# Performance work log

Hardware: AMD Instinct MI355X
Metric: run time of the kernel (lower is better)

The kernel has to match this reference:

```python
import math
import jax, jax.numpy as jnp
import numpy as np

N_HEADS = 8
EPS = 1e-6


def setup_inputs() -> dict:
    key = jax.random.key(0)
    k0, k1, k2, k3, k4 = jax.random.split(key, 5)
    B, T, E = 2, 1024, 512
    s = 1.0 / math.sqrt(E)
    x = jax.random.normal(k0, (B, T, E), dtype=jnp.float32)
    w_qkv = jax.random.normal(k1, (3 * E, E), dtype=jnp.float32) * s
    b_qkv = jax.random.normal(k2, (3 * E,), dtype=jnp.float32) * s
    w_out = jax.random.normal(k3, (E, E), dtype=jnp.float32) * s
    b_out = jax.random.normal(k4, (E,), dtype=jnp.float32) * s
    return {"x": x, "w_qkv": w_qkv, "b_qkv": b_qkv, "w_out": w_out, "b_out": b_out}


def reference(x, w_qkv, b_qkv, w_out, b_out):
    B, T, C = x.shape
    H = N_HEADS
    d = C // H

    qkv = x @ w_qkv.T + b_qkv                      # [B,T,3C]
    q, k, v = jnp.split(qkv, 3, axis=-1)

    def to_heads(t):
        return t.reshape(B, T, H, d).transpose(0, 2, 1, 3).astype(jnp.float32)  # [B,H,T,d]

    q, k, v = to_heads(q), to_heads(k), to_heads(v)

    pos = jnp.arange(T, dtype=jnp.float32)
    ang = (math.pi / 2) * pos / T
    cos_w = jnp.cos(ang)[None, None, :, None]      # [1,1,T,1]
    sin_w = jnp.sin(ang)[None, None, :, None]

    q_prime = jax.nn.relu(q)
    k_prime = jax.nn.relu(k)
    q_cos, q_sin = q_prime * cos_w, q_prime * sin_w
    k_cos, k_sin = k_prime * cos_w, k_prime * sin_w

    # causal linear attention via cumulative outer products (cosFormer)
    kv_cos_cs = jnp.cumsum(jnp.einsum('bhtd,bhte->bhtde', k_cos, v), axis=2)
    context = jnp.einsum('bhtd,bhtde->bhte', q_cos, kv_cos_cs)
    kv_sin_cs = jnp.cumsum(jnp.einsum('bhtd,bhte->bhtde', k_sin, v), axis=2)
    context = context + jnp.einsum('bhtd,bhtde->bhte', q_sin, kv_sin_cs)

    norm = (jnp.einsum('bhtd,bhtd->bht', q_cos, jnp.cumsum(k_cos, axis=2))
            + jnp.einsum('bhtd,bhtd->bht', q_sin, jnp.cumsum(k_sin, axis=2)))
    out = context / (norm[..., None] + EPS)        # [B,H,T,d]

    out = out.astype(x.dtype).transpose(0, 2, 1, 3).reshape(B, T, C)
    return out @ w_out.T + b_out
```

## Files before the change

kernel.cpp:

```cpp
#include <hip/hip_runtime.h>

typedef __bf16 bf16_t;
typedef __bf16 bf16x4 __attribute__((ext_vector_type(4)));
typedef __bf16 bf16x8 __attribute__((ext_vector_type(8)));
typedef float f32x4 __attribute__((ext_vector_type(4)));

#define T_SEQ 1024
#define EMB   512
#define NH    8
#define HD    64
#define BATCH 2
#define NBH   (BATCH*NH)
#define CHUNK 64
#define NCHUNK (T_SEQ/CHUNK)
#define NBLK  (NBH*NCHUNK)
#define LDA   72


__global__ __launch_bounds__(256) void cvt3_kernel(
    const float* __restrict__ x, const float* __restrict__ wq,
    const float* __restrict__ wo,
    bf16_t* __restrict__ xb, bf16_t* __restrict__ wqb, bf16_t* __restrict__ wob)
{
    int i = blockIdx.x * 256 + threadIdx.x;
    const float* s; bf16_t* d; int off;
    if (i < 262144)      { s = x;  d = xb;  off = i; }
    else if (i < 458752) { s = wq; d = wqb; off = i - 262144; }
    else                 { s = wo; d = wob; off = i - 458752; }
    float4 v = ((const float4*)s)[off];
    bf16x4 o;
    o[0] = (bf16_t)v.x; o[1] = (bf16_t)v.y;
    o[2] = (bf16_t)v.z; o[3] = (bf16_t)v.w;
    ((bf16x4*)d)[off] = o;
}

__global__ __launch_bounds__(64) void qkv_gemm_kernel(
    const bf16_t* __restrict__ X, const bf16_t* __restrict__ W,
    const float* __restrict__ bias,
    bf16_t* __restrict__ qq, bf16_t* __restrict__ kk, bf16_t* __restrict__ vv)
{
    const int lane = threadIdx.x;
    const int rsel = lane & 15;
    const int koff = (lane >> 4) * 8;
    const int m0 = blockIdx.x * 64;
    const int n0 = blockIdx.y * 64;
    f32x4 acc[4][4] = {};
    const bf16_t* Ap = X + (m0 + rsel) * EMB + koff;
    const bf16_t* Bp = W + (n0 + rsel) * EMB + koff;
#pragma unroll 4
    for (int k0 = 0; k0 < EMB; k0 += 32) {
        bf16x8 af[4], bfr[4];
        for (int i = 0; i < 4; ++i)
            af[i] = *(const bf16x8*)(Ap + i * 16 * EMB + k0);
        for (int j = 0; j < 4; ++j)
            bfr[j] = *(const bf16x8*)(Bp + j * 16 * EMB + k0);
        for (int i = 0; i < 4; ++i)
            for (int j = 0; j < 4; ++j)
                acc[i][j] = __builtin_amdgcn_mfma_f32_16x16x32_bf16(
                    af[i], bfr[j], acc[i][j], 0, 0, 0);
    }
    for (int j = 0; j < 4; ++j) {
        const int n = n0 + j * 16 + rsel;
        const float bn = bias[n];
        const int sec = n >> 9;
        const int c = n & 511;
        const int h = c >> 6, e = c & 63;
        for (int i = 0; i < 4; ++i) {
            const int mb = m0 + i * 16 + (lane >> 4) * 4;
            for (int r = 0; r < 4; ++r) {
                int m = mb + r;
                int b = m >> 10, t = m & 1023;
                float val = acc[i][j][r] + bn;
                int di = ((b * NH + h) * T_SEQ + t) * HD + e;
                if (sec == 0) {
                    qq[di] = (bf16_t)fmaxf(val, 0.f);
                } else if (sec == 1) {
                    kk[di] = (bf16_t)fmaxf(val, 0.f);
                } else {
                    vv[di] = (bf16_t)val;
                }
            }
        }
    }
}

__global__ __launch_bounds__(256) void chunk_sum_kernel(
    const bf16_t* __restrict__ kk, const bf16_t* __restrict__ vv,
    bf16_t* __restrict__ Ssc, bf16_t* __restrict__ Sss,
    float* __restrict__ zc, float* __restrict__ zs)
{
    const int blk = blockIdx.x;
    const int ch = blk & 15;
    __shared__ __align__(16) bf16_t sk[CHUNK * HD];
    __shared__ __align__(16) bf16_t sv[CHUNK * HD];
    __shared__ float cwt[CHUNK], swt[CHUNK];
    const int base = blk * CHUNK * HD;
    for (int i = threadIdx.x; i < CHUNK * HD / 8; i += 256) {
        ((uint4*)sk)[i] = ((const uint4*)(kk + base))[i];
        ((uint4*)sv)[i] = ((const uint4*)(vv + base))[i];
    }
    if (threadIdx.x < CHUNK) {
        int tg = ch * CHUNK + threadIdx.x;
        float ang = 1.5707963267948966f * (float)tg * (1.0f / (float)T_SEQ);
        cwt[threadIdx.x] = cosf(ang);
        swt[threadIdx.x] = sinf(ang);
    }
    __syncthreads();
    const int i  = threadIdx.x & 63;
    const int jg = (threadIdx.x >> 6) * 16;
    float ac[16], as[16];
    for (int jj = 0; jj < 16; ++jj) { ac[jj] = 0.f; as[jj] = 0.f; }
    float zca = 0.f, zsa = 0.f;
    const bool zown = (jg == 0);
    for (int t = 0; t < CHUNK; ++t) {
        float kv = (float)sk[t * HD + i];
        float kc_ = kv * cwt[t];
        float ks_ = kv * swt[t];
        if (zown) { zca += kc_; zsa += ks_; }
        for (int jj = 0; jj < 16; ++jj) {
            float vj = (float)sv[t * HD + jg + jj];
            ac[jj] += kc_ * vj;
            as[jj] += ks_ * vj;
        }
    }
    bf16_t* oc = Ssc + blk * HD * HD;
    bf16_t* os = Sss + blk * HD * HD;
    for (int jj = 0; jj < 16; ++jj) {
        oc[(jg + jj) * HD + i] = (bf16_t)ac[jj];
        os[(jg + jj) * HD + i] = (bf16_t)as[jj];
    }
    if (zown) {
        zc[blk * HD + i] = zca;
        zs[blk * HD + i] = zsa;
    }
}

__global__ __launch_bounds__(256) void chunk_out_kernel(
    const bf16_t* __restrict__ qq, const bf16_t* __restrict__ kk,
    const bf16_t* __restrict__ vv,
    const bf16_t* __restrict__ SscT, const bf16_t* __restrict__ SssT,
    const float* __restrict__ zc, const float* __restrict__ zs,
    bf16_t* __restrict__ Y)
{
    const int blk = blockIdx.x;
    const int bh = blk >> 4, ch = blk & 15;
    __shared__ __align__(16) bf16_t sq [CHUNK * LDA];
    __shared__ __align__(16) bf16_t sk [CHUNK * LDA];
    __shared__ __align__(16) bf16_t svT[CHUNK * LDA];
    __shared__ __align__(16) bf16_t sct[CHUNK * LDA];
    __shared__ __align__(16) bf16_t sst[CHUNK * LDA];
    __shared__ __align__(16) bf16_t sp [CHUNK * LDA];
    __shared__ float cwt[CHUNK], swt[CHUNK], cosd[CHUNK];
    __shared__ float zcl[CHUNK], zsl[CHUNK], nrm[CHUNK];

    const int base = blk * CHUNK * HD;
    for (int i = threadIdx.x; i < CHUNK * HD / 8; i += 256) {
        int row = i >> 3, g = i & 7;
        ((uint4*)(sq + row * LDA))[g]  = ((const uint4*)(qq + base))[i];
        ((uint4*)(sk + row * LDA))[g]  = ((const uint4*)(kk + base))[i];
        bf16x8 v8 = *(const bf16x8*)(vv + base + i * 8);
        int t = i >> 3, b = i & 7;
        int tg8 = t >> 3, tf = t & 7;
        for (int j = 0; j < 8; ++j) {
            int e = b * 8 + j;
            int pg = (tg8 + b) & 7;
            svT[e * LDA + pg * 8 + tf] = v8[j];
        }
    }
    {
        const int e0 = threadIdx.x * 16;
        float accC[16], accS[16];
        for (int j = 0; j < 16; ++j) { accC[j] = 0.f; accS[j] = 0.f; }
        const int sb = bh * NCHUNK * HD * HD + e0;
#pragma unroll 2
        for (int c = 0; c < ch; ++c) {
            const bf16x8* pc = (const bf16x8*)(SscT + sb + c * HD * HD);
            const bf16x8* ps = (const bf16x8*)(SssT + sb + c * HD * HD);
            bf16x8 c0 = pc[0], c1 = pc[1], s0 = ps[0], s1 = ps[1];
            for (int j = 0; j < 8; ++j) {
                accC[j] += (float)c0[j];  accC[8 + j] += (float)c1[j];
                accS[j] += (float)s0[j];  accS[8 + j] += (float)s1[j];
            }
        }
        const int row = threadIdx.x >> 2, col = (threadIdx.x & 3) * 16;
        bf16x8 oc0, oc1, os0, os1;
        for (int j = 0; j < 8; ++j) {
            oc0[j] = (bf16_t)accC[j];  oc1[j] = (bf16_t)accC[8 + j];
            os0[j] = (bf16_t)accS[j];  os1[j] = (bf16_t)accS[8 + j];
        }
        *(bf16x8*)(sct + row * LDA + col) = oc0;
        *(bf16x8*)(sct + row * LDA + col + 8) = oc1;
        *(bf16x8*)(sst + row * LDA + col) = os0;
        *(bf16x8*)(sst + row * LDA + col + 8) = os1;
    }
    if (threadIdx.x < HD) {
        int tl = threadIdx.x;
        float s = 0.f;
        for (int c = 0; c < ch; ++c) s += zc[(bh * NCHUNK + c) * HD + tl];
        zcl[tl] = s;
        int tg = ch * CHUNK + tl;
        float angg = 1.5707963267948966f * (float)tg * (1.0f / (float)T_SEQ);
        cwt[tl] = cosf(angg);
        swt[tl] = sinf(angg);
        cosd[tl] = cosf(1.5707963267948966f * (float)tl * (1.0f / (float)T_SEQ));
    } else if (threadIdx.x < 2 * HD) {
        int i = threadIdx.x - HD;
        float s = 0.f;
        for (int c = 0; c < ch; ++c) s += zs[(bh * NCHUNK + c) * HD + i];
        zsl[i] = s;
    }
    __syncthreads();

    const int w = threadIdx.x >> 6;
    const int lane = threadIdx.x & 63;
    const int rsel = lane & 15;
    const int koff = (lane >> 4) * 8;
    const int myrow = w * 16 + rsel;

    bf16x8 aq0 = *(const bf16x8*)(sq + myrow * LDA + koff);
    bf16x8 aq1 = *(const bf16x8*)(sq + myrow * LDA + koff + 32);
    for (int nt = 0; nt < 4; ++nt) {
        const int n0 = nt * 16;
        f32x4 pacc = {0.f, 0.f, 0.f, 0.f};
        bf16x8 b0 = *(const bf16x8*)(sk + (n0 + rsel) * LDA + koff);
        bf16x8 b1 = *(const bf16x8*)(sk + (n0 + rsel) * LDA + koff + 32);
        pacc = __builtin_amdgcn_mfma_f32_16x16x32_bf16(aq0, b0, pacc, 0, 0, 0);
        pacc = __builtin_amdgcn_mfma_f32_16x16x32_bf16(aq1, b1, pacc, 0, 0, 0);
        const int s = n0 + (lane & 15);
        const int tb = w * 16 + (lane >> 4) * 4;
        for (int r = 0; r < 4; ++r) {
            int t = tb + r;
            float p = (s <= t) ? pacc[r] * cosd[t - s] : 0.f;
            sp[t * LDA + s] = (bf16_t)p;
        }
    }

    if (lane < 16) {
        int row = w * 16 + lane;
        float nv = 0.f;
        const bf16x8* pr = (const bf16x8*)(sp + row * LDA);
        for (int g = 0; g < 8; ++g) {
            bf16x8 pv = pr[g];
            for (int j = 0; j < 8; ++j) nv += (float)pv[j];
        }
        float cwr = cwt[row], swr = swt[row];
        const bf16x8* qr = (const bf16x8*)(sq + row * LDA);
        for (int g = 0; g < 8; ++g) {
            bf16x8 qv = qr[g];
            for (int j = 0; j < 8; ++j)
                nv += (float)qv[j] * (cwr * zcl[g * 8 + j] + swr * zsl[g * 8 + j]);
        }
        nrm[row] = nv;
    }

    const float cwq = cwt[myrow], swq = swt[myrow];
    bf16x8 qc0, qc1, qs0, qs1;
    for (int j = 0; j < 8; ++j) {
        qc0[j] = (bf16_t)((float)aq0[j] * cwq);
        qc1[j] = (bf16_t)((float)aq1[j] * cwq);
        qs0[j] = (bf16_t)((float)aq0[j] * swq);
        qs1[j] = (bf16_t)((float)aq1[j] * swq);
    }
    bf16x8 ap0 = *(const bf16x8*)(sp + myrow * LDA + koff);
    bf16x8 ap1 = *(const bf16x8*)(sp + myrow * LDA + koff + 32);

    const int b = bh >> 3, h = bh & 7;
    const int g0 = koff >> 3;
    for (int nt = 0; nt < 4; ++nt) {
        const int n0 = nt * 16;
        const int ee = n0 + rsel;
        const int rot = (ee >> 3) & 7;
        const bf16_t* bvp0 = svT + ee * LDA + (((g0 + rot) & 7) << 3);
        const bf16_t* bvp1 = svT + ee * LDA + (((g0 + 4 + rot) & 7) << 3);
        const bf16_t* bcp = sct + ee * LDA + koff;
        const bf16_t* bsp = sst + ee * LDA + koff;
        f32x4 acc = {0.f, 0.f, 0.f, 0.f};
        acc = __builtin_amdgcn_mfma_f32_16x16x32_bf16(ap0, *(const bf16x8*)(bvp0), acc, 0, 0, 0);
        acc = __builtin_amdgcn_mfma_f32_16x16x32_bf16(ap1, *(const bf16x8*)(bvp1), acc, 0, 0, 0);
        acc = __builtin_amdgcn_mfma_f32_16x16x32_bf16(qc0, *(const bf16x8*)(bcp), acc, 0, 0, 0);
        acc = __builtin_amdgcn_mfma_f32_16x16x32_bf16(qc1, *(const bf16x8*)(bcp + 32), acc, 0, 0, 0);
        acc = __builtin_amdgcn_mfma_f32_16x16x32_bf16(qs0, *(const bf16x8*)(bsp), acc, 0, 0, 0);
        acc = __builtin_amdgcn_mfma_f32_16x16x32_bf16(qs1, *(const bf16x8*)(bsp + 32), acc, 0, 0, 0);
        const int col = n0 + (lane & 15);
        const int tb = w * 16 + (lane >> 4) * 4;
        for (int r = 0; r < 4; ++r) {
            int row = tb + r;
            float inv = 1.0f / (nrm[row] + 1e-6f);
            int tg = ch * CHUNK + row;
            Y[((b * T_SEQ + tg) * EMB) + h * HD + col] = (bf16_t)(acc[r] * inv);
        }
    }
}

__global__ __launch_bounds__(256) void out_gemm_kernel(
    const bf16_t* __restrict__ Yb, const bf16_t* __restrict__ W,
    const float* __restrict__ bias, float* __restrict__ out)
{
    const int w = threadIdx.x >> 6;
    const int lane = threadIdx.x & 63;
    const int rsel = lane & 15;
    const int koff = (lane >> 4) * 8;
    const int m0 = blockIdx.x * 64 + (w & 1) * 32;
    const int n0 = blockIdx.y * 64 + (w >> 1) * 32;
    f32x4 acc[2][2] = {};
    const bf16_t* Ap = Yb + (m0 + rsel) * EMB + koff;
    const bf16_t* Bp = W + (n0 + rsel) * EMB + koff;
#pragma unroll 8
    for (int k0 = 0; k0 < EMB; k0 += 32) {
        bf16x8 af[2], bfr[2];
        for (int i = 0; i < 2; ++i)
            af[i] = *(const bf16x8*)(Ap + i * 16 * EMB + k0);
        for (int j = 0; j < 2; ++j)
            bfr[j] = *(const bf16x8*)(Bp + j * 16 * EMB + k0);
        for (int i = 0; i < 2; ++i)
            for (int j = 0; j < 2; ++j)
                acc[i][j] = __builtin_amdgcn_mfma_f32_16x16x32_bf16(
                    af[i], bfr[j], acc[i][j], 0, 0, 0);
    }
    for (int j = 0; j < 2; ++j) {
        const int n = n0 + j * 16 + rsel;
        const float bn = bias[n];
        for (int i = 0; i < 2; ++i) {
            const int mb = m0 + i * 16 + (lane >> 4) * 4;
            for (int r = 0; r < 4; ++r)
                out[(mb + r) * EMB + n] = acc[i][j][r] + bn;
        }
    }
}

extern "C" void kernel_launch(void* const* d_in, const int* in_sizes, int n_in,
                              void* d_out, int out_size, void* d_ws, size_t ws_size,
                              hipStream_t stream) {
    const float* x     = (const float*)d_in[0];
    const float* w_qkv = (const float*)d_in[1];
    const float* b_qkv = (const float*)d_in[2];
    const float* w_out = (const float*)d_in[3];
    const float* b_out = (const float*)d_in[4];
    float* out = (float*)d_out;

    char* w = (char*)d_ws;
    const size_t N_X   = (size_t)BATCH * T_SEQ * EMB;
    const size_t N_WQ  = (size_t)3 * EMB * EMB;
    const size_t N_WO  = (size_t)EMB * EMB;
    bf16_t* xb   = (bf16_t*)w;                 w += N_X  * sizeof(bf16_t);
    bf16_t* wqb  = (bf16_t*)w;                 w += N_WQ * sizeof(bf16_t);
    bf16_t* wob  = (bf16_t*)w;                 w += N_WO * sizeof(bf16_t);
    const size_t SZ_BHTD = (size_t)NBH * T_SEQ * HD * sizeof(bf16_t);
    bf16_t* qq = (bf16_t*)w;                   w += SZ_BHTD;
    bf16_t* kk = (bf16_t*)w;                   w += SZ_BHTD;
    bf16_t* vv = (bf16_t*)w;                   w += SZ_BHTD;
    bf16_t* Y  = (bf16_t*)w;                   w += SZ_BHTD;
    bf16_t* SscT = (bf16_t*)w;                 w += (size_t)NBLK * HD * HD * sizeof(bf16_t);
    bf16_t* SssT = (bf16_t*)w;                 w += (size_t)NBLK * HD * HD * sizeof(bf16_t);
    float* zc = (float*)w;                     w += (size_t)NBLK * HD * sizeof(float);
    float* zs = (float*)w;

    cvt3_kernel<<<2048, 256, 0, stream>>>(x, w_qkv, w_out, xb, wqb, wob);
    qkv_gemm_kernel<<<dim3(2048 / 64, 1536 / 64), 64, 0, stream>>>(
        xb, wqb, b_qkv, qq, kk, vv);
    chunk_sum_kernel<<<NBLK, 256, 0, stream>>>(kk, vv, SscT, SssT, zc, zs);
    chunk_out_kernel<<<NBLK, 256, 0, stream>>>(qq, kk, vv, SscT, SssT, zc, zs, Y);
    out_gemm_kernel<<<dim3(2048 / 64, 512 / 64), 256, 0, stream>>>(
        Y, wob, b_out, out);
}
```

Before: 119.5 us.

## Fuse QKV projection GEMM with per-chunk KV state summation kernel

Merges the QKV GEMM and the chunk-sum kernel into one 256-thread block per (64-row tile, head). Three waves compute the Q, K and V tiles for that head, and the K and V results go straight into padded shared memory for the chunk outer-product sum. This removes one kernel launch and the global re-read of K and V. In exchange, the fourth wave idles during the GEMM, the grid shrinks from 768 single-wave blocks to 256 four-wave blocks, and the blocks are heavier.

Result: no change. 118.0 us (-1.2%).

```diff
diff --git a/kernel.cpp b/kernel.cpp
--- a/kernel.cpp
+++ b/kernel.cpp
@@ -15,6 +15,7 @@
 #define NCHUNK (T_SEQ/CHUNK)
 #define NBLK  (NBH*NCHUNK)
 #define LDA   72
+#define LDK   68
 
 
 __global__ __launch_bounds__(256) void cvt3_kernel(
@@ -34,78 +35,78 @@
     ((bf16x4*)d)[off] = o;
 }
 
-__global__ __launch_bounds__(64) void qkv_gemm_kernel(
+__global__ __launch_bounds__(256) void qkv_sum_kernel(
     const bf16_t* __restrict__ X, const bf16_t* __restrict__ W,
     const float* __restrict__ bias,
-    bf16_t* __restrict__ qq, bf16_t* __restrict__ kk, bf16_t* __restrict__ vv)
-{
-    const int lane = threadIdx.x;
-    const int rsel = lane & 15;
-    const int koff = (lane >> 4) * 8;
-    const int m0 = blockIdx.x * 64;
-    const int n0 = blockIdx.y * 64;
-    f32x4 acc[4][4] = {};
-    const bf16_t* Ap = X + (m0 + rsel) * EMB + koff;
-    const bf16_t* Bp = W + (n0 + rsel) * EMB + koff;
-#pragma unroll 4
-    for (int k0 = 0; k0 < EMB; k0 += 32) {
-        bf16x8 af[4], bfr[4];
-        for (int i = 0; i < 4; ++i)
-            af[i] = *(const bf16x8*)(Ap + i * 16 * EMB + k0);
-        for (int j = 0; j < 4; ++j)
-            bfr[j] = *(const bf16x8*)(Bp + j * 16 * EMB + k0);
-        for (int i = 0; i < 4; ++i)
-            for (int j = 0; j < 4; ++j)
-                acc[i][j] = __builtin_amdgcn_mfma_f32_16x16x32_bf16(
-                    af[i], bfr[j], acc[i][j], 0, 0, 0);
-    }
-    for (int j = 0; j < 4; ++j) {
-        const int n = n0 + j * 16 + rsel;
-        const float bn = bias[n];
-        const int sec = n >> 9;
-        const int c = n & 511;
-        const int h = c >> 6, e = c & 63;
-        for (int i = 0; i < 4; ++i) {
-            const int mb = m0 + i * 16 + (lane >> 4) * 4;
-            for (int r = 0; r < 4; ++r) {
-                int m = mb + r;
-                int b = m >> 10, t = m & 1023;
-                float val = acc[i][j][r] + bn;
-                int di = ((b * NH + h) * T_SEQ + t) * HD + e;
-                if (sec == 0) {
-                    qq[di] = (bf16_t)fmaxf(val, 0.f);
-                } else if (sec == 1) {
-                    kk[di] = (bf16_t)fmaxf(val, 0.f);
-                } else {
-                    vv[di] = (bf16_t)val;
-                }
-            }
-        }
-    }
-}
-
-__global__ __launch_bounds__(256) void chunk_sum_kernel(
-    const bf16_t* __restrict__ kk, const bf16_t* __restrict__ vv,
+    bf16_t* __restrict__ qq, bf16_t* __restrict__ kk, bf16_t* __restrict__ vv,
     bf16_t* __restrict__ Ssc, bf16_t* __restrict__ Sss,
     float* __restrict__ zc, float* __restrict__ zs)
 {
-    const int blk = blockIdx.x;
-    const int ch = blk & 15;
-    __shared__ __align__(16) bf16_t sk[CHUNK * HD];
-    __shared__ __align__(16) bf16_t sv[CHUNK * HD];
+    __shared__ __align__(16) bf16_t sk[CHUNK * LDK];
+    __shared__ __align__(16) bf16_t sv[CHUNK * LDK];
     __shared__ float cwt[CHUNK], swt[CHUNK];
-    const int base = blk * CHUNK * HD;
-    for (int i = threadIdx.x; i < CHUNK * HD / 8; i += 256) {
-        ((uint4*)sk)[i] = ((const uint4*)(kk + base))[i];
-        ((uint4*)sv)[i] = ((const uint4*)(vv + base))[i];
-    }
+
+    const int m0 = blockIdx.x * 64;
+    const int h  = blockIdx.y;
+    const int b  = m0 >> 10;
+    const int ch = (m0 & 1023) >> 6;
+    const int blk = (b * NH + h) * NCHUNK + ch;
+
     if (threadIdx.x < CHUNK) {
         int tg = ch * CHUNK + threadIdx.x;
         float ang = 1.5707963267948966f * (float)tg * (1.0f / (float)T_SEQ);
         cwt[threadIdx.x] = cosf(ang);
         swt[threadIdx.x] = sinf(ang);
     }
+
+    const int w = threadIdx.x >> 6;
+    const int lane = threadIdx.x & 63;
+    if (w < 3) {
+        const int rsel = lane & 15;
+        const int koff = (lane >> 4) * 8;
+        const int n0 = w * 512 + h * 64;
+        f32x4 acc[4][4] = {};
+        const bf16_t* Ap = X + (m0 + rsel) * EMB + koff;
+        const bf16_t* Bp = W + (n0 + rsel) * EMB + koff;
+#pragma unroll 4
+        for (int k0 = 0; k0 < EMB; k0 += 32) {
+            bf16x8 af[4], bfr[4];
+            for (int i = 0; i < 4; ++i)
+                af[i] = *(const bf16x8*)(Ap + i * 16 * EMB + k0);
+            for (int j = 0; j < 4; ++j)
+                bfr[j] = *(const bf16x8*)(Bp + j * 16 * EMB + k0);
+            for (int i = 0; i < 4; ++i)
+                for (int j = 0; j < 4; ++j)
+                    acc[i][j] = __builtin_amdgcn_mfma_f32_16x16x32_bf16(
+                        af[i], bfr[j], acc[i][j], 0, 0, 0);
+        }
+        for (int j = 0; j < 4; ++j) {
+            const int feat = j * 16 + rsel;
+            const float bn = bias[n0 + feat];
+            for (int i = 0; i < 4; ++i) {
+                const int tl0 = i * 16 + (lane >> 4) * 4;
+                for (int r = 0; r < 4; ++r) {
+                    const int tl = tl0 + r;
+                    const int t = (m0 & 1023) + tl;
+                    float val = acc[i][j][r] + bn;
+                    int di = ((b * NH + h) * T_SEQ + t) * HD + feat;
+                    if (w == 0) {
+                        qq[di] = (bf16_t)fmaxf(val, 0.f);
+                    } else if (w == 1) {
+                        bf16_t kb = (bf16_t)fmaxf(val, 0.f);
+                        kk[di] = kb;
+                        sk[tl * LDK + feat] = kb;
+                    } else {
+                        bf16_t vb = (bf16_t)val;
+                        vv[di] = vb;
+                        sv[tl * LDK + feat] = vb;
+                    }
+                }
+            }
+        }
+    }
     __syncthreads();
+
     const int i  = threadIdx.x & 63;
     const int jg = (threadIdx.x >> 6) * 16;
     float ac[16], as[16];
@@ -113,12 +114,12 @@
     float zca = 0.f, zsa = 0.f;
     const bool zown = (jg == 0);
     for (int t = 0; t < CHUNK; ++t) {
-        float kv = (float)sk[t * HD + i];
+        float kv = (float)sk[t * LDK + i];
         float kc_ = kv * cwt[t];
         float ks_ = kv * swt[t];
         if (zown) { zca += kc_; zsa += ks_; }
         for (int jj = 0; jj < 16; ++jj) {
-            float vj = (float)sv[t * HD + jg + jj];
+            float vj = (float)sv[t * LDK + jg + jj];
             ac[jj] += kc_ * vj;
             as[jj] += ks_ * vj;
         }
@@ -159,11 +160,11 @@
         ((uint4*)(sq + row * LDA))[g]  = ((const uint4*)(qq + base))[i];
         ((uint4*)(sk + row * LDA))[g]  = ((const uint4*)(kk + base))[i];
         bf16x8 v8 = *(const bf16x8*)(vv + base + i * 8);
-        int t = i >> 3, b = i & 7;
+        int t = i >> 3, bb = i & 7;
         int tg8 = t >> 3, tf = t & 7;
         for (int j = 0; j < 8; ++j) {
-            int e = b * 8 + j;
-            int pg = (tg8 + b) & 7;
+            int e = bb * 8 + j;
+            int pg = (tg8 + bb) & 7;
             svT[e * LDA + pg * 8 + tf] = v8[j];
         }
     }
@@ -356,9 +357,8 @@
     float* zs = (float*)w;
 
     cvt3_kernel<<<2048, 256, 0, stream>>>(x, w_qkv, w_out, xb, wqb, wob);
-    qkv_gemm_kernel<<<dim3(2048 / 64, 1536 / 64), 64, 0, stream>>>(
-        xb, wqb, b_qkv, qq, kk, vv);
-    chunk_sum_kernel<<<NBLK, 256, 0, stream>>>(kk, vv, SscT, SssT, zc, zs);
+    qkv_sum_kernel<<<dim3(32, 8), 256, 0, stream>>>(
+        xb, wqb, b_qkv, qq, kk, vv, SscT, SssT, zc, zs);
     chunk_out_kernel<<<NBLK, 256, 0, stream>>>(qq, kk, vv, SscT, SssT, zc, zs, Y);
     out_gemm_kernel<<<dim3(2048 / 64, 512 / 64), 256, 0, stream>>>(
         Y, wob, b_out, out);
```
